# Optimization experiments

Measured on AMD Instinct MI355X. Metric: run time of the kernel, lower is better.

The kernel has to match this reference:

```python
import jax, jax.numpy as jnp
import numpy as np

D = 1024   # d_model
H = 16     # n_heads
S = 2048   # seq_len
HD = D // H  # head_dim = 64
B = 1


def setup_inputs() -> dict:
    key = jax.random.key(0)
    ks = jax.random.split(key, 10)
    s = 0.02
    return {
        "x": jax.random.normal(ks[0], (B, S * D), dtype=jnp.float32),
        "Wq": jax.random.normal(ks[1], (D, D), dtype=jnp.float32) * s,
        "bq": jnp.zeros((D,), dtype=jnp.float32),
        "Wk": jax.random.normal(ks[2], (D, D), dtype=jnp.float32) * s,
        "bk": jnp.zeros((D,), dtype=jnp.float32),
        "Wv": jax.random.normal(ks[3], (D, D), dtype=jnp.float32) * s,
        "bv": jnp.zeros((D,), dtype=jnp.float32),
        "Wo": jax.random.normal(ks[4], (D, D), dtype=jnp.float32) * s,
        "bo": jnp.zeros((D,), dtype=jnp.float32),
        "rel_table": jax.random.normal(ks[5], (2 * S - 1, HD), dtype=jnp.float32),
    }


def reference(x, Wq, bq, Wk, bk, Wv, bv, Wo, bo, rel_table):
    b = x.shape[0]
    x3 = x.reshape(b, S, D)
    # projections; split into heads -> [b, H, S, HD]
    def heads(t):
        return t.reshape(b, S, H, HD).transpose(0, 2, 1, 3)
    Q = heads(x3 @ Wq + bq)
    K = heads(x3 @ Wk + bk)
    V = heads(x3 @ Wv + bv)

    scores = jnp.einsum('bhid,bhjd->bhij', Q, K) / np.sqrt(HD).astype(np.float32)

    # relative position index: clamp(i - j + S - 1, 0, 2S-2)
    pos = jnp.arange(S)
    idx = jnp.clip(pos[:, None] - pos[None, :] + S - 1, 0, 2 * S - 2)  # [S, S]
    # contract Q with the raw table once, then gather per (i, j)
    # (same math as einsum('bhid,ijd->bhij', Q, table[idx]) but avoids [S,S,HD])
    qrel = jnp.einsum('bhid,rd->bhir', Q, rel_table)          # [b, H, S, 2S-1]
    rel_scores = jnp.take_along_axis(qrel, idx[None, None, :, :], axis=-1)  # [b,H,S,S]

    attn = jax.nn.softmax(scores + rel_scores, axis=-1)
    # dropout is identity in eval mode
    out = jnp.einsum('bhij,bhjd->bhid', attn, V)              # [b, H, S, HD]
    out = out.transpose(0, 2, 1, 3).reshape(b, S, D)
    return (out @ Wo + bo).reshape(b, -1)
```

## Files before the change

### kernel.cpp

```cpp
#include <hip/hip_runtime.h>
#include <hip/hip_bf16.h>

#define SEQ 2048
#define DM  1024
#define NH  16
#define HDM 64

typedef __hip_bfloat16 bf16;
typedef __bf16 bhalf8 __attribute__((ext_vector_type(8)));
typedef float floatx4 __attribute__((ext_vector_type(4)));

__device__ __forceinline__ void async_cp16(const void* g, void* l) {
  __builtin_amdgcn_global_load_lds(
      (const __attribute__((address_space(1))) void*)g,
      (__attribute__((address_space(3))) void*)l, 16, 0, 0);
}

__global__ __launch_bounds__(256) void prep(
    const float* __restrict__ x, const float* __restrict__ T,
    const float* __restrict__ W0, const float* __restrict__ W1,
    const float* __restrict__ W2, const float* __restrict__ W3,
    bf16* __restrict__ xbf, bf16* __restrict__ Tbf, bf16* __restrict__ WtBase)
{
  __shared__ float tile[64][69];
  const int b = blockIdx.x;
  const int tid = threadIdx.x;
  if (b < 2048) {
    int c = b * 256 + tid;
    float4 v = *(const float4*)&x[(size_t)c * 4];
    union { bf16 h[4]; float2 f; } u;
    u.h[0] = __float2bfloat16(v.x); u.h[1] = __float2bfloat16(v.y);
    u.h[2] = __float2bfloat16(v.z); u.h[3] = __float2bfloat16(v.w);
    *(float2*)&xbf[(size_t)c * 4] = u.f;
  } else if (b < 2304) {
    int ct = (b - 2048) * 256 + tid;
    union { bf16 h[4]; float2 f; } u;
#pragma unroll
    for (int e = 0; e < 4; ++e) {
      int se = ct * 4 + e;
      if (se >= 4095 * 64) se -= 64;
      u.h[e] = __float2bfloat16(T[se]);
    }
    *(float2*)&Tbf[(size_t)ct * 4] = u.f;
  } else {
    int tb = b - 2304;
    int z = tb >> 8, rem = tb & 255;
    const float* W = (z == 0) ? W0 : (z == 1) ? W1 : (z == 2) ? W2 : W3;
    bf16* Wt = WtBase + (size_t)z * DM * DM;
    const int kb = (rem >> 4) * 64, nb = (rem & 15) * 64;
    const int r = tid >> 4, c4 = (tid & 15) * 4;
#pragma unroll
    for (int rr = 0; rr < 4; ++rr) {
      float4 v = *(const float4*)&W[(size_t)(kb + rr * 16 + r) * DM + nb + c4];
      tile[rr * 16 + r][c4 + 0] = v.x; tile[rr * 16 + r][c4 + 1] = v.y;
      tile[rr * 16 + r][c4 + 2] = v.z; tile[rr * 16 + r][c4 + 3] = v.w;
    }
    __syncthreads();
    const int w = tid >> 6, l = tid & 63;
#pragma unroll
    for (int i = 0; i < 16; ++i) {
      int n = nb + w * 16 + i;
      Wt[(size_t)n * DM + kb + l] = __float2bfloat16(tile[l][w * 16 + i]);
    }
  }
}

__device__ __forceinline__ void gemm64_core(
    const bf16* __restrict__ A, const bf16* __restrict__ Bt,
    bf16* As, bf16* Bs, int bm, int bn, floatx4 (&acc)[4])
{
  const int tid = threadIdx.x;
  const int lane = tid & 63;
  const int w = tid >> 6;
  const int ln15 = lane & 15, quad = lane >> 4;
  const int qs8  = (quad ^ ((ln15 >> 1) & 3)) * 8;
  const int srow = tid >> 2;
  const int scol = ((tid & 3) ^ ((tid >> 3) & 3)) * 8;

  for (int k0 = 0; k0 < DM; k0 += 64) {
    async_cp16(A  + (size_t)(bm + srow) * DM + k0 + scol,      As + tid * 8);
    async_cp16(A  + (size_t)(bm + srow) * DM + k0 + 32 + scol, As + 2048 + tid * 8);
    async_cp16(Bt + (size_t)(bn + srow) * DM + k0 + scol,      Bs + tid * 8);
    async_cp16(Bt + (size_t)(bn + srow) * DM + k0 + 32 + scol, Bs + 2048 + tid * 8);
    __syncthreads();
#pragma unroll
    for (int kk = 0; kk < 2; ++kk) {
      bhalf8 af = *(bhalf8*)&As[kk * 2048 + (w * 16 + ln15) * 32 + qs8];
      bhalf8 bfr[4];
#pragma unroll
      for (int j = 0; j < 4; ++j)
        bfr[j] = *(bhalf8*)&Bs[kk * 2048 + (j * 16 + ln15) * 32 + qs8];
#pragma unroll
      for (int j = 0; j < 4; ++j)
        acc[j] = __builtin_amdgcn_mfma_f32_16x16x32_bf16(af, bfr[j], acc[j], 0, 0, 0);
    }
    __syncthreads();
  }
}

__global__ __launch_bounds__(256) void gemm_qkv128(
    const bf16* __restrict__ A, const bf16* __restrict__ Wt3,
    const float* __restrict__ bq, const float* __restrict__ bk,
    const float* __restrict__ bv, bf16* __restrict__ outbase)
{
  __shared__ __align__(16) bf16 As[128 * 64];
  __shared__ __align__(16) bf16 Bs[128 * 64];
  const int z = blockIdx.z;
  const bf16* Bt = Wt3 + (size_t)z * DM * DM;
  const float* bias = (z == 0) ? bq : (z == 1) ? bk : bv;
  const float kscale = (z == 1) ? 0.125f : 1.0f;
  bf16* C = outbase + (size_t)z * SEQ * DM;
  const int bm = blockIdx.y * 128, bn = blockIdx.x * 128;
  const int tid = threadIdx.x;
  const int lane = tid & 63, w = tid >> 6;
  const int ln15 = lane & 15, quad = lane >> 4;
  const int wr = (w >> 1) * 64, wc = (w & 1) * 64;

  floatx4 acc[4][4];
#pragma unroll
  for (int mi = 0; mi < 4; ++mi)
#pragma unroll
    for (int nj = 0; nj < 4; ++nj) acc[mi][nj] = (floatx4){0.f, 0.f, 0.f, 0.f};

  for (int k0 = 0; k0 < DM; k0 += 64) {
#pragma unroll
    for (int t = 0; t < 4; ++t) {
      int cid = t * 256 + tid;
      int row = cid >> 3;
      int scol = ((cid & 7) ^ (row & 7)) * 8;
      async_cp16(A  + (size_t)(bm + row) * DM + k0 + scol, As + cid * 8);
      async_cp16(Bt + (size_t)(bn + row) * DM + k0 + scol, Bs + cid * 8);
    }
    __syncthreads();
#pragma unroll
    for (int kk = 0; kk < 2; ++kk) {
      const int chs = ((kk * 4 + quad) ^ (ln15 & 7)) * 8;
      bhalf8 af[4], bfr[4];
#pragma unroll
      for (int mi = 0; mi < 4; ++mi)
        af[mi] = *(bhalf8*)&As[(wr + mi * 16 + ln15) * 64 + chs];
#pragma unroll
      for (int nj = 0; nj < 4; ++nj)
        bfr[nj] = *(bhalf8*)&Bs[(wc + nj * 16 + ln15) * 64 + chs];
#pragma unroll
      for (int mi = 0; mi < 4; ++mi)
#pragma unroll
        for (int nj = 0; nj < 4; ++nj)
          acc[mi][nj] = __builtin_amdgcn_mfma_f32_16x16x32_bf16(
              af[mi], bfr[nj], acc[mi][nj], 0, 0, 0);
    }
    __syncthreads();
  }

#pragma unroll
  for (int nj = 0; nj < 4; ++nj) {
    int col = bn + wc + nj * 16 + ln15;
    float bv_ = bias[col];
#pragma unroll
    for (int mi = 0; mi < 4; ++mi) {
#pragma unroll
      for (int r = 0; r < 4; ++r) {
        int row = bm + wr + mi * 16 + quad * 4 + r;
        float v = (acc[mi][nj][r] + bv_) * kscale;
        if (z < 2)
          C[((size_t)(col >> 6) * SEQ + row) * HDM + (col & 63)] = __float2bfloat16(v);
        else
          C[(size_t)col * SEQ + row] = __float2bfloat16(v);
      }
    }
  }
}

__global__ __launch_bounds__(256) void gemm_out(
    const bf16* __restrict__ A, const bf16* __restrict__ Bt,
    const float* __restrict__ bias, float* __restrict__ C)
{
  __shared__ __align__(16) bf16 As[64 * 64];
  __shared__ __align__(16) bf16 Bs[64 * 64];
  const int bm = blockIdx.y * 64, bn = blockIdx.x * 64;
  floatx4 acc[4];
#pragma unroll
  for (int j = 0; j < 4; ++j) acc[j] = (floatx4){0.f, 0.f, 0.f, 0.f};
  gemm64_core(A, Bt, As, Bs, bm, bn, acc);

  const int lane = threadIdx.x & 63;
  const int w = threadIdx.x >> 6;
  const int ln15 = lane & 15, quad = lane >> 4;
#pragma unroll
  for (int j = 0; j < 4; ++j) {
    int col = bn + j * 16 + ln15;
    float bv_ = bias[col];
#pragma unroll
    for (int r = 0; r < 4; ++r) {
      int row = bm + w * 16 + quad * 4 + r;
      C[(size_t)row * DM + col] = acc[j][r] + bv_;
    }
  }
}

__global__ __launch_bounds__(256, 2) void attn_flash(
    const bf16* __restrict__ Q, const bf16* __restrict__ K,
    const bf16* __restrict__ Vt, const bf16* __restrict__ Tb,
    bf16* __restrict__ Opart, float* __restrict__ lws)
{
  const int i0   = blockIdx.x * 64;
  const int h    = blockIdx.y;
  const int z    = blockIdx.z;
  const int tid  = threadIdx.x;
  const int lane = tid & 63;
  const int wrow = (tid >> 6) * 16;
  const int ln15 = lane & 15;
  const int quad = lane >> 4;

  __shared__ __align__(16) unsigned char smem[75264];
  bf16*  Ps  = (bf16*)(smem + 49152);
  float* S2c = (float*)(smem + 58368);
  bf16*  Qs  = (bf16*)(smem + 58368);

  const bf16* Qg = Q  + ((size_t)h * SEQ + i0) * HDM;
  const bf16* Kg = K  + (size_t)h * SEQ * HDM;
  const bf16* Vg = Vt + (size_t)h * HDM * SEQ;

  const int r4 = tid >> 2;
  const int c8s = (((tid & 3) ^ ((r4 >> 1) & 3)) * 8);
  auto stage = [&](int jt_, int b) {
    int j0_ = jt_ * 64;
    int rb_ = i0 - j0_ + SEQ - HDM;
    bf16* Kd = (bf16*)smem + b * 4096;
    bf16* Vd = (bf16*)smem + 8192 + b * 4096;
    bf16* Td = (bf16*)smem + 16384 + b * 4096;
    async_cp16(Kg + (size_t)(j0_ + r4) * HDM + c8s,        Kd + tid * 8);
    async_cp16(Kg + (size_t)(j0_ + r4) * HDM + 32 + c8s,   Kd + 2048 + tid * 8);
    async_cp16(Vg + (size_t)r4 * SEQ + j0_ + c8s,          Vd + tid * 8);
    async_cp16(Vg + (size_t)r4 * SEQ + j0_ + 32 + c8s,     Vd + 2048 + tid * 8);
    async_cp16(Tb + (size_t)(rb_ + r4) * HDM + c8s,        Td + tid * 8);
    async_cp16(Tb + (size_t)(rb_ + r4) * HDM + 32 + c8s,   Td + 2048 + tid * 8);
  };

  const int jt0 = z * 16;
  stage(jt0, 0);

#pragma unroll
  for (int t = 0; t < 2; ++t) {
    int id = tid + t * 256;
    int r = id >> 3, c = (id & 7) * 8;
    *(float4*)&Qs[r * 72 + c] = *(const float4*)&Qg[(size_t)r * HDM + c];
  }
  __syncthreads();

  const bhalf8 aq0 = *(bhalf8*)&Qs[(wrow + ln15) * 72 + quad * 8];
  const bhalf8 aq1 = *(bhalf8*)&Qs[(wrow + ln15) * 72 + quad * 8 + 32];

  floatx4 o[4];
  float lsum[4];
#pragma unroll
  for (int c = 0; c < 4; ++c) { o[c] = (floatx4){0.f, 0.f, 0.f, 0.f}; lsum[c] = 0.f; }

  const int rb0 = i0 - jt0 * 64 + SEQ - HDM;
  floatx4 carry[4];
#pragma unroll
  for (int ct = 0; ct < 4; ++ct) {
    const bf16* tr = Tb + (size_t)(rb0 + 64 + ct * 16 + ln15) * HDM + quad * 8;
    bhalf8 b0 = *(const bhalf8*)tr;
    bhalf8 b1 = *(const bhalf8*)(tr + 32);
    floatx4 a = (floatx4){0.f, 0.f, 0.f, 0.f};
    a = __builtin_amdgcn_mfma_f32_16x16x32_bf16(aq0, b0, a, 0, 0, 0);
    a = __builtin_amdgcn_mfma_f32_16x16x32_bf16(aq1, b1, a, 0, 0, 0);
    carry[ct] = a;
  }

  const int qsw = (quad ^ ((ln15 >> 1) & 3)) * 8;
  const int pc0 = (quad ^ (ln15 >> 1)) * 8;
  const int pc1 = pc0 ^ 32;
  const int prow = wrow + ln15;

  int cur = 0;
  for (int jt = jt0; jt < jt0 + 16; ++jt) {
    __syncthreads();
    if (jt + 1 < jt0 + 16) stage(jt + 1, cur ^ 1);
    const bf16* Ksc = (bf16*)smem + cur * 4096;
    const bf16* Vsc = (bf16*)smem + 8192 + cur * 4096;
    const bf16* Tsc = (bf16*)smem + 16384 + cur * 4096;

    floatx4 fresh[4];
#pragma unroll
    for (int ct = 0; ct < 4; ++ct) {
      bhalf8 b0 = *(bhalf8*)&Tsc[(ct * 16 + ln15) * 32 + qsw];
      bhalf8 b1 = *(bhalf8*)&Tsc[2048 + (ct * 16 + ln15) * 32 + qsw];
      floatx4 a = (floatx4){0.f, 0.f, 0.f, 0.f};
      a = __builtin_amdgcn_mfma_f32_16x16x32_bf16(aq0, b0, a, 0, 0, 0);
      a = __builtin_amdgcn_mfma_f32_16x16x32_bf16(aq1, b1, a, 0, 0, 0);
      fresh[ct] = a;
    }
#pragma unroll
    for (int ct = 0; ct < 4; ++ct) {
      int t = ct * 16 + ln15;
#pragma unroll
      for (int r = 0; r < 4; ++r) {
        int row = wrow + quad * 4 + r;
        if (t >= row) S2c[row * 66 + (row + 63 - t)] = fresh[ct][r];
        else          S2c[row * 66 + (row - 1 - t)] = carry[ct][r];
      }
      carry[ct] = fresh[ct];
    }

#pragma unroll
    for (int ct = 0; ct < 4; ++ct) {
      floatx4 s2f;
#pragma unroll
      for (int r = 0; r < 4; ++r)
        s2f[r] = S2c[(wrow + quad * 4 + r) * 66 + ct * 16 + ln15];
      bhalf8 b0 = *(bhalf8*)&Ksc[(ct * 16 + ln15) * 32 + qsw];
      bhalf8 b1 = *(bhalf8*)&Ksc[2048 + (ct * 16 + ln15) * 32 + qsw];
      floatx4 a = __builtin_amdgcn_mfma_f32_16x16x32_bf16(aq0, b0, s2f, 0, 0, 0);
      a = __builtin_amdgcn_mfma_f32_16x16x32_bf16(aq1, b1, a, 0, 0, 0);
#pragma unroll
      for (int r = 0; r < 4; ++r) {
        float p = __expf(a[r]);
        lsum[r] += p;
        int row = wrow + quad * 4 + r;
        int pch = ((ct * 2 + (ln15 >> 3)) ^ ((row >> 1) & 7)) * 8;
        Ps[row * 64 + pch + (ln15 & 7)] = __float2bfloat16(p);
      }
    }

    bhalf8 ap0 = *(bhalf8*)&Ps[prow * 64 + pc0];
    bhalf8 ap1 = *(bhalf8*)&Ps[prow * 64 + pc1];
#pragma unroll
    for (int ct = 0; ct < 4; ++ct) {
      bhalf8 b0 = *(bhalf8*)&Vsc[(ct * 16 + ln15) * 32 + qsw];
      bhalf8 b1 = *(bhalf8*)&Vsc[2048 + (ct * 16 + ln15) * 32 + qsw];
      o[ct] = __builtin_amdgcn_mfma_f32_16x16x32_bf16(ap0, b0, o[ct], 0, 0, 0);
      o[ct] = __builtin_amdgcn_mfma_f32_16x16x32_bf16(ap1, b1, o[ct], 0, 0, 0);
    }
    cur ^= 1;
  }

  bf16* Oz = Opart + (size_t)z * SEQ * DM;
#pragma unroll
  for (int r = 0; r < 4; ++r) {
    float l = lsum[r];
    l += __shfl_xor(l, 1); l += __shfl_xor(l, 2);
    l += __shfl_xor(l, 4); l += __shfl_xor(l, 8);
    float inv = 1.f / l;
    int row = i0 + wrow + quad * 4 + r;
#pragma unroll
    for (int ct = 0; ct < 4; ++ct)
      Oz[(size_t)row * DM + h * HDM + ct * 16 + ln15] =
          __float2bfloat16(o[ct][r] * inv);
    if (ln15 == 0)
      lws[((size_t)z * NH + h) * SEQ + row] = l;
  }
}

__global__ __launch_bounds__(256) void attn_merge(
    const bf16* __restrict__ O0, const bf16* __restrict__ O1,
    const float* __restrict__ lws, bf16* __restrict__ O)
{
  const int i = blockIdx.x;
  const int tid = threadIdx.x;
  __shared__ float w0s[NH], w1s[NH];
  if (tid < NH) {
    float l0 = lws[((size_t)0 * NH + tid) * SEQ + i];
    float l1 = lws[((size_t)1 * NH + tid) * SEQ + i];
    float inv = 1.f / (l0 + l1);
    w0s[tid] = l0 * inv; w1s[tid] = l1 * inv;
  }
  __syncthreads();
  const int d = tid * 4;
  const float w0 = w0s[d >> 6], w1 = w1s[d >> 6];
  union { bf16 h[4]; float2 f; } a0, a1, ov;
  a0.f = *(const float2*)&O0[(size_t)i * DM + d];
  a1.f = *(const float2*)&O1[(size_t)i * DM + d];
#pragma unroll
  for (int e = 0; e < 4; ++e)
    ov.h[e] = __float2bfloat16(w0 * __bfloat162float(a0.h[e]) +
                               w1 * __bfloat162float(a1.h[e]));
  *(float2*)&O[(size_t)i * DM + d] = ov.f;
}

extern "C" void kernel_launch(void* const* d_in, const int* in_sizes, int n_in,
                              void* d_out, int out_size, void* d_ws, size_t ws_size,
                              hipStream_t stream) {
  const float* x   = (const float*)d_in[0];
  const float* Wq  = (const float*)d_in[1];
  const float* bq  = (const float*)d_in[2];
  const float* Wk  = (const float*)d_in[3];
  const float* bk  = (const float*)d_in[4];
  const float* Wv  = (const float*)d_in[5];
  const float* bv  = (const float*)d_in[6];
  const float* Wo  = (const float*)d_in[7];
  const float* bo  = (const float*)d_in[8];
  const float* rel = (const float*)d_in[9];
  float* out = (float*)d_out;

  const size_t SD = (size_t)SEQ * DM;
  bf16* qws = (bf16*)d_ws;
  bf16* kws = qws + SD;
  bf16* vws = kws + SD;
  bf16* ows = vws + SD;
  bf16* xbf = ows + SD;
  bf16* wt  = xbf + SD;
  bf16* tbf = wt + 4 * (size_t)DM * DM;
  bf16* opart = tbf + (size_t)4096 * HDM;
  float* lws  = (float*)(opart + 2 * SD);

  prep<<<3328, 256, 0, stream>>>(x, rel, Wq, Wk, Wv, Wo, xbf, tbf, wt);
  gemm_qkv128<<<dim3(8, 16, 3), 256, 0, stream>>>(xbf, wt, bq, bk, bv, qws);
  attn_flash<<<dim3(SEQ / 64, NH, 2), 256, 0, stream>>>(qws, kws, vws, tbf,
                                                        opart, lws);
  attn_merge<<<SEQ, 256, 0, stream>>>(opart, opart + SD, lws, ows);
  gemm_out<<<dim3(16, 32), 256, 0, stream>>>(ows, wt + 3 * (size_t)DM * DM, bo, out);
}
```

Measured before the change: 200.6 us.

## Shrink attention LDS footprint to fit three blocks per CU

The rel-table tile is no longer staged through LDS; it is read straight from global memory each iteration. Q fragments are loaded directly from global instead of through a shared staging buffer. The S2 and P scratch areas are merged into a per-wave slab that is reused in place, with all S2 values read into registers before P overwrites them. Together these cut shared memory from about 75KB to about 50KB so launch bounds can request three blocks per CU. The cost is uncoalesced global reads of the table on the critical path, plus higher register pressure from the larger occupancy target.

```diff
diff --git a/kernel.cpp b/kernel.cpp
--- a/kernel.cpp
+++ b/kernel.cpp
@@ -198,7 +198,7 @@
   }
 }
 
-__global__ __launch_bounds__(256, 2) void attn_flash(
+__global__ __launch_bounds__(256, 3) void attn_flash(
     const bf16* __restrict__ Q, const bf16* __restrict__ K,
     const bf16* __restrict__ Vt, const bf16* __restrict__ Tb,
     bf16* __restrict__ Opart, float* __restrict__ lws)
@@ -208,14 +208,15 @@
   const int z    = blockIdx.z;
   const int tid  = threadIdx.x;
   const int lane = tid & 63;
-  const int wrow = (tid >> 6) * 16;
+  const int w    = tid >> 6;
+  const int wrow = w * 16;
   const int ln15 = lane & 15;
   const int quad = lane >> 4;
 
-  __shared__ __align__(16) unsigned char smem[75264];
-  bf16*  Ps  = (bf16*)(smem + 49152);
-  float* S2c = (float*)(smem + 58368);
-  bf16*  Qs  = (bf16*)(smem + 58368);
+  __shared__ __align__(16) unsigned char smem[50176];
+  unsigned char* slab = smem + 32768 + w * 4352;
+  float* S2w = (float*)slab;
+  bf16*  Psw = (bf16*)slab;
 
   const bf16* Qg = Q  + ((size_t)h * SEQ + i0) * HDM;
   const bf16* Kg = K  + (size_t)h * SEQ * HDM;
@@ -225,31 +226,19 @@
   const int c8s = (((tid & 3) ^ ((r4 >> 1) & 3)) * 8);
   auto stage = [&](int jt_, int b) {
     int j0_ = jt_ * 64;
-    int rb_ = i0 - j0_ + SEQ - HDM;
     bf16* Kd = (bf16*)smem + b * 4096;
     bf16* Vd = (bf16*)smem + 8192 + b * 4096;
-    bf16* Td = (bf16*)smem + 16384 + b * 4096;
     async_cp16(Kg + (size_t)(j0_ + r4) * HDM + c8s,        Kd + tid * 8);
     async_cp16(Kg + (size_t)(j0_ + r4) * HDM + 32 + c8s,   Kd + 2048 + tid * 8);
     async_cp16(Vg + (size_t)r4 * SEQ + j0_ + c8s,          Vd + tid * 8);
     async_cp16(Vg + (size_t)r4 * SEQ + j0_ + 32 + c8s,     Vd + 2048 + tid * 8);
-    async_cp16(Tb + (size_t)(rb_ + r4) * HDM + c8s,        Td + tid * 8);
-    async_cp16(Tb + (size_t)(rb_ + r4) * HDM + 32 + c8s,   Td + 2048 + tid * 8);
   };
 
   const int jt0 = z * 16;
   stage(jt0, 0);
 
-#pragma unroll
-  for (int t = 0; t < 2; ++t) {
-    int id = tid + t * 256;
-    int r = id >> 3, c = (id & 7) * 8;
-    *(float4*)&Qs[r * 72 + c] = *(const float4*)&Qg[(size_t)r * HDM + c];
-  }
-  __syncthreads();
-
-  const bhalf8 aq0 = *(bhalf8*)&Qs[(wrow + ln15) * 72 + quad * 8];
-  const bhalf8 aq1 = *(bhalf8*)&Qs[(wrow + ln15) * 72 + quad * 8 + 32];
+  const bhalf8 aq0 = *(const bhalf8*)&Qg[(size_t)(wrow + ln15) * HDM + quad * 8];
+  const bhalf8 aq1 = *(const bhalf8*)&Qg[(size_t)(wrow + ln15) * HDM + quad * 8 + 32];
 
   floatx4 o[4];
   float lsum[4];
@@ -272,21 +261,22 @@
   const int qsw = (quad ^ ((ln15 >> 1) & 3)) * 8;
   const int pc0 = (quad ^ (ln15 >> 1)) * 8;
   const int pc1 = pc0 ^ 32;
-  const int prow = wrow + ln15;
 
   int cur = 0;
   for (int jt = jt0; jt < jt0 + 16; ++jt) {
+    const int j0 = jt * 64;
+    const int rb = i0 - j0 + SEQ - HDM;
     __syncthreads();
     if (jt + 1 < jt0 + 16) stage(jt + 1, cur ^ 1);
     const bf16* Ksc = (bf16*)smem + cur * 4096;
     const bf16* Vsc = (bf16*)smem + 8192 + cur * 4096;
-    const bf16* Tsc = (bf16*)smem + 16384 + cur * 4096;
 
     floatx4 fresh[4];
 #pragma unroll
     for (int ct = 0; ct < 4; ++ct) {
-      bhalf8 b0 = *(bhalf8*)&Tsc[(ct * 16 + ln15) * 32 + qsw];
-      bhalf8 b1 = *(bhalf8*)&Tsc[2048 + (ct * 16 + ln15) * 32 + qsw];
+      const bf16* tr = Tb + (size_t)(rb + ct * 16 + ln15) * HDM + quad * 8;
+      bhalf8 b0 = *(const bhalf8*)tr;
+      bhalf8 b1 = *(const bhalf8*)(tr + 32);
       floatx4 a = (floatx4){0.f, 0.f, 0.f, 0.f};
       a = __builtin_amdgcn_mfma_f32_16x16x32_bf16(aq0, b0, a, 0, 0, 0);
       a = __builtin_amdgcn_mfma_f32_16x16x32_bf16(aq1, b1, a, 0, 0, 0);
@@ -298,34 +288,39 @@
 #pragma unroll
       for (int r = 0; r < 4; ++r) {
         int row = wrow + quad * 4 + r;
-        if (t >= row) S2c[row * 66 + (row + 63 - t)] = fresh[ct][r];
-        else          S2c[row * 66 + (row - 1 - t)] = carry[ct][r];
+        int lr = quad * 4 + r;
+        if (t >= row) S2w[lr * 68 + (row + 63 - t)] = fresh[ct][r];
+        else          S2w[lr * 68 + (row - 1 - t)] = carry[ct][r];
       }
       carry[ct] = fresh[ct];
     }
 
+    float s2f[4][4];
+#pragma unroll
+    for (int ct = 0; ct < 4; ++ct)
+#pragma unroll
+      for (int r = 0; r < 4; ++r)
+        s2f[ct][r] = S2w[(quad * 4 + r) * 68 + ct * 16 + ln15];
+
 #pragma unroll
     for (int ct = 0; ct < 4; ++ct) {
-      floatx4 s2f;
-#pragma unroll
-      for (int r = 0; r < 4; ++r)
-        s2f[r] = S2c[(wrow + quad * 4 + r) * 66 + ct * 16 + ln15];
+      floatx4 cva = {s2f[ct][0], s2f[ct][1], s2f[ct][2], s2f[ct][3]};
       bhalf8 b0 = *(bhalf8*)&Ksc[(ct * 16 + ln15) * 32 + qsw];
       bhalf8 b1 = *(bhalf8*)&Ksc[2048 + (ct * 16 + ln15) * 32 + qsw];
-      floatx4 a = __builtin_amdgcn_mfma_f32_16x16x32_bf16(aq0, b0, s2f, 0, 0, 0);
+      floatx4 a = __builtin_amdgcn_mfma_f32_16x16x32_bf16(aq0, b0, cva, 0, 0, 0);
       a = __builtin_amdgcn_mfma_f32_16x16x32_bf16(aq1, b1, a, 0, 0, 0);
 #pragma unroll
       for (int r = 0; r < 4; ++r) {
         float p = __expf(a[r]);
         lsum[r] += p;
-        int row = wrow + quad * 4 + r;
-        int pch = ((ct * 2 + (ln15 >> 3)) ^ ((row >> 1) & 7)) * 8;
-        Ps[row * 64 + pch + (ln15 & 7)] = __float2bfloat16(p);
+        int lr = quad * 4 + r;
+        int pch = ((ct * 2 + (ln15 >> 3)) ^ ((lr >> 1) & 7)) * 8;
+        Psw[lr * 136 + pch + (ln15 & 7)] = __float2bfloat16(p);
       }
     }
 
-    bhalf8 ap0 = *(bhalf8*)&Ps[prow * 64 + pc0];
-    bhalf8 ap1 = *(bhalf8*)&Ps[prow * 64 + pc1];
+    bhalf8 ap0 = *(bhalf8*)&Psw[ln15 * 136 + pc0];
+    bhalf8 ap1 = *(bhalf8*)&Psw[ln15 * 136 + pc1];
 #pragma unroll
     for (int ct = 0; ct < 4; ++ct) {
       bhalf8 b0 = *(bhalf8*)&Vsc[(ct * 16 + ln15) * 32 + qsw];
```

Result: slower. 237.3 us (+18.3%).
